# Performance work log

Measured on AMD Instinct MI355X. Metric: run time of the kernel, lower is better.

The kernel has to match this reference:

```python
import jax, jax.numpy as jnp
import numpy as np

N, E, D_IN, D_E, H, OUT, L = 16384, 131072, 128, 64, 256, 16, 4
EPS_MSG = 1e-7   # GENConv message epsilon
EPS_SM = 1e-16   # PyG softmax denominator epsilon


def _ln(x, g, b, eps=1e-5):
    mu = x.mean(-1, keepdims=True)
    var = x.var(-1, keepdims=True)
    return (x - mu) * jax.lax.rsqrt(var + eps) * g + b


def _genconv(x, src, dst, e, w1, b1, lng, lnb, w2, b2, t):
    # message: relu(x_j + edge_attr) + eps  -> [E, H]
    msg = jax.nn.relu(x[src] + e) + EPS_MSG
    # learnable-temperature segment softmax over incoming edges, per feature
    m = msg * t
    mx = jax.ops.segment_max(m, dst, num_segments=N)
    mx = jnp.where(jnp.isfinite(mx), mx, 0.0)  # empty segments -> 0
    ex = jnp.exp(m - mx[dst])
    den = jax.ops.segment_sum(ex, dst, num_segments=N)
    alpha = ex / (den[dst] + EPS_SM)
    agg = jax.ops.segment_sum(msg * alpha, dst, num_segments=N)  # [N, H]
    # root residual then 2-layer MLP: Linear -> LayerNorm -> ReLU -> Linear
    out = agg + x
    h = jax.nn.relu(_ln(out @ w1 + b1, lng, lnb))
    return h @ w2 + b2


def setup_inputs() -> dict:
    key = jax.random.key(0)
    ks = jax.random.split(key, 10)
    gl = lambda k, shape, fan: jax.random.normal(k, shape, jnp.float32) / np.sqrt(fan).astype(np.float32)
    return {
        "x": jax.random.normal(ks[0], (N, D_IN), jnp.float32),
        "edge_index": jax.random.randint(ks[1], (2, E), 0, N, dtype=jnp.int32),
        "edge_attr": jax.random.normal(ks[2], (E, D_E), jnp.float32),
        "enc_w": gl(ks[3], (D_IN, H), D_IN), "enc_b": jnp.zeros((H,), jnp.float32),
        "ee_w": gl(ks[4], (D_E, H), D_E), "ee_b": jnp.zeros((H,), jnp.float32),
        "w1": gl(ks[5], (L, H, 2 * H), H), "b1": jnp.zeros((L, 2 * H), jnp.float32),
        "lng": jnp.ones((L, 2 * H), jnp.float32), "lnb": jnp.zeros((L, 2 * H), jnp.float32),
        "w2": gl(ks[6], (L, 2 * H, H), 2 * H), "b2": jnp.zeros((L, H), jnp.float32),
        "t": jnp.ones((L,), jnp.float32),
        "ng": jnp.ones((L, H), jnp.float32), "nb": jnp.zeros((L, H), jnp.float32),
        "lin_w": gl(ks[7], (H, OUT), H), "lin_b": jnp.zeros((OUT,), jnp.float32),
    }


def reference(x, edge_index, edge_attr, enc_w, enc_b, ee_w, ee_b,
              w1, b1, lng, lnb, w2, b2, t, ng, nb, lin_w, lin_b):
    src, dst = edge_index[0], edge_index[1]
    h = x @ enc_w + enc_b                      # node encoder
    e = edge_attr @ ee_w + ee_b                # edge encoder
    # first layer: conv only (per source forward)
    h = _genconv(h, src, dst, e, w1[0], b1[0], lng[0], lnb[0], w2[0], b2[0], t[0])
    # remaining layers: res+ block = x + conv(relu(norm(x)))  (dropout off in eval)
    for i in range(1, L):
        z = jax.nn.relu(_ln(h, ng[i], nb[i]))
        h = h + _genconv(z, src, dst, e, w1[i], b1[i], lng[i], lnb[i], w2[i], b2[i], t[i])
    h = jax.nn.relu(_ln(h, ng[0], nb[0]))      # layers[0].act(layers[0].norm(x))
    return h @ lin_w + lin_b
```

## Files before the change

kernel.cpp:

```cpp
#include <hip/hip_runtime.h>
#include <stdint.h>
#include <math.h>


typedef __bf16 bf16x8 __attribute__((ext_vector_type(8)));
typedef __bf16 bf16x4 __attribute__((ext_vector_type(4)));
typedef float  f32x4  __attribute__((ext_vector_type(4)));

constexpr int NN   = 16384;
constexpr int NE   = 131072;
constexpr int DIN  = 128;
constexpr int DE   = 64;
constexpr int HD   = 256;
constexpr int HD2  = 512;

__device__ __forceinline__ void gl_lds16(const __bf16* g, __bf16* l) {
  __builtin_amdgcn_global_load_lds((const __attribute__((address_space(1))) void*)g,
                                   (__attribute__((address_space(3))) void*)l, 16, 0, 0);
}

__global__ __launch_bounds__(1024) void k_scan(const int* __restrict__ deg,
                                               int* __restrict__ row_start) {
  __shared__ int part[1024];
  const int t = threadIdx.x;
  const int base = t * 16;
  int loc[16];
  int s = 0;
  #pragma unroll
  for (int i = 0; i < 16; i++) { loc[i] = s; s += deg[base + i]; }
  part[t] = s;
  __syncthreads();
  for (int off = 1; off < 1024; off <<= 1) {
    int v = (t >= off) ? part[t - off] : 0;
    __syncthreads();
    part[t] += v;
    __syncthreads();
  }
  const int excl = (t == 0) ? 0 : part[t - 1];
  #pragma unroll
  for (int i = 0; i < 16; i++) row_start[base + i] = excl + loc[i];
}

__global__ void k_scatter(const int* __restrict__ src, const int* __restrict__ dst,
                          const int* __restrict__ row_start, int* __restrict__ cursor,
                          int2* __restrict__ csr_es) {
  int e = blockIdx.x * 256 + threadIdx.x;
  if (e >= NE) return;
  const int d = dst[e];
  const int p = atomicAdd(&cursor[d], 1);
  csr_es[row_start[d] + p] = make_int2(e, src[e]);
}

__global__ __launch_bounds__(256)
void k_sortw(const int* __restrict__ row_start, const int* __restrict__ deg,
             int2* __restrict__ csr_es, int* __restrict__ posmap) {
  const int wv   = threadIdx.x >> 6;
  const int lane = threadIdx.x & 63;
  const int node = blockIdx.x * 4 + wv;
  if (node >= NN) return;
  const int st = __builtin_amdgcn_readfirstlane(row_start[node]);
  const int dg = __builtin_amdgcn_readfirstlane(deg[node]);
  if (dg <= 1) {
    if (dg == 1 && lane == 0) posmap[csr_es[st].x] = st;
    return;
  }
  if (dg <= 64) {
    int2 pr = make_int2(0x7fffffff, 0);
    if (lane < dg) pr = csr_es[st + lane];
    int rank = 0;
    for (int j = 0; j < dg; j++) {
      const int ej = __builtin_amdgcn_readlane(pr.x, j);
      if (lane < dg && ej < pr.x) rank++;
    }
    if (lane < dg) {
      csr_es[st + rank] = pr;
      posmap[pr.x] = st + rank;
    }
  } else if (lane == 0) {
    for (int a = 1; a < dg; a++) {
      int2 k = csr_es[st + a];
      int b = a - 1;
      while (b >= 0 && csr_es[st + b].x > k.x) { csr_es[st + b + 1] = csr_es[st + b]; b--; }
      csr_es[st + b + 1] = k;
    }
    for (int a = 0; a < dg; a++) posmap[csr_es[st + a].x] = st + a;
  }
}

__global__ void k_prep(const float* __restrict__ enc_w, const float* __restrict__ ee_w,
                       const float* __restrict__ w1, const float* __restrict__ w2,
                       const int* __restrict__ dst, int* __restrict__ deg,
                       __bf16* __restrict__ enc_wT, __bf16* __restrict__ ee_wT,
                       __bf16* __restrict__ w1T, __bf16* __restrict__ w2T) {
  int i = blockIdx.x * 256 + threadIdx.x;
  const int S0 = DIN * HD, S1 = DE * HD, S2 = 4 * HD * HD2, S3 = 4 * HD2 * HD;
  if (i < S0) { int k = i / HD, n = i % HD; enc_wT[n * DIN + k] = (__bf16)enc_w[i]; return; }
  i -= S0;
  if (i < S1) { int k = i / HD, n = i % HD; ee_wT[n * DE + k] = (__bf16)ee_w[i]; return; }
  i -= S1;
  if (i < S2) {
    int l = i / (HD * HD2), r = i % (HD * HD2), k = r / HD2, n = r % HD2;
    w1T[(size_t)l * HD * HD2 + (size_t)n * HD + k] = (__bf16)w1[i]; return;
  }
  i -= S2;
  if (i < S3) {
    int l = i / (HD2 * HD), r = i % (HD2 * HD), k = r / HD, n = r % HD;
    w2T[(size_t)l * HD2 * HD + (size_t)n * HD2 + k] = (__bf16)w2[i]; return;
  }
  i -= S3;
  if (i < NE) { atomicAdd(&deg[dst[i]], 1); return; }
}

template <int RES, int OBF, int STATS, int ESCAT, int AF32>
__global__ __launch_bounds__(256, 3)
void k_gemm(const void* __restrict__ Ap, const __bf16* __restrict__ BT,
            const float* __restrict__ bias, const float* __restrict__ R,
            float* __restrict__ Cf, __bf16* __restrict__ Cb,
            const int* __restrict__ posmap, float2* __restrict__ pstats,
            int M, int Nn, int K) {
  __shared__ __attribute__((aligned(16))) char smem[49152];
  float (*sm)[129] = (float(*)[129])smem;
  float* sbias     = (float*)(smem + 16512);
  float2 (*pst4)[32] = (float2(*)[32])(smem + 17024);
  const __bf16* Ab = (const __bf16*)Ap;
  const float*  Af = (const float*)Ap;
  const int tid  = threadIdx.x;
  const int lane = tid & 63;
  const int wave = tid >> 6;
  const int ntn  = Nn >> 7;
  const int bid  = (int)blockIdx.x;
  const int bn   = (bid >> 3) % ntn;
  const int bm   = (bid & 7) + ((bid >> 3) / ntn) * 8;
  const size_t row0 = (size_t)bm * 128, col0 = (size_t)bn * 128;
  const int wr = (wave >> 1) * 64, wc = (wave & 1) * 64;
  const int ks = lane >> 4, fr = lane & 15;

  auto bufA = [&](int i) -> __bf16* { return (__bf16*)(smem + i * 8192); };
  auto bufB = [&](int i) -> __bf16* { return (__bf16*)(smem + 24576 + i * 8192); };

  f32x4 acc[4][4] = {};

  const int arow = tid >> 2;
  const int aksg = (tid & 3) ^ ((arow >> 1) & 3);

  auto stageB = [&](__bf16* lb, int k0) {
    gl_lds16(BT + (col0 + arow) * K + k0 + aksg * 8, &lb[tid * 8]);
    gl_lds16(BT + (col0 + arow + 64) * K + k0 + aksg * 8, &lb[(tid + 256) * 8]);
  };
  auto stageA = [&](__bf16* la, int k0) {
    gl_lds16(Ab + (row0 + arow) * K + k0 + aksg * 8, &la[tid * 8]);
    gl_lds16(Ab + (row0 + arow + 64) * K + k0 + aksg * 8, &la[(tid + 256) * 8]);
  };
  float4 p0, p1, q0, q1;
  auto loadAf = [&](int k0) {
    const float* a0p = &Af[(row0 + arow) * K + k0 + aksg * 8];
    const float* a1p = &Af[(row0 + arow + 64) * K + k0 + aksg * 8];
    p0 = *(const float4*)a0p; p1 = *(const float4*)(a0p + 4);
    q0 = *(const float4*)a1p; q1 = *(const float4*)(a1p + 4);
  };
  auto writeAf = [&](__bf16* la) {
    bf16x8 o0, o1;
    o0[0] = (__bf16)p0.x; o0[1] = (__bf16)p0.y; o0[2] = (__bf16)p0.z; o0[3] = (__bf16)p0.w;
    o0[4] = (__bf16)p1.x; o0[5] = (__bf16)p1.y; o0[6] = (__bf16)p1.z; o0[7] = (__bf16)p1.w;
    o1[0] = (__bf16)q0.x; o1[1] = (__bf16)q0.y; o1[2] = (__bf16)q0.z; o1[3] = (__bf16)q0.w;
    o1[4] = (__bf16)q1.x; o1[5] = (__bf16)q1.y; o1[6] = (__bf16)q1.z; o1[7] = (__bf16)q1.w;
    *(bf16x8*)&la[tid * 8] = o0;
    *(bf16x8*)&la[(tid + 256) * 8] = o1;
  };

  int slA[4], slB[4];
  #pragma unroll
  for (int m = 0; m < 4; m++) {
    const int rm = wr + m * 16 + fr;
    slA[m] = rm * 4 + (ks ^ ((rm >> 1) & 3));
    const int cn = wc + m * 16 + fr;
    slB[m] = cn * 4 + (ks ^ ((cn >> 1) & 3));
  }

  const int nk = K / 32;
  if (AF32) { loadAf(0); stageB(bufB(0), 0); writeAf(bufA(0)); }
  else      { stageA(bufA(0), 0); stageB(bufB(0), 0); }
  if (nk > 1) {
    if (AF32) { loadAf(32); stageB(bufB(1), 32); writeAf(bufA(1)); }
    else      { stageA(bufA(1), 32); stageB(bufB(1), 32); }
  }
  for (int t = 0; t < nk; t++) {
    const int rem = nk - 1 - t;
    const int nb3 = (t + 2) % 3;
    if (rem >= 2) {
      if (AF32) { loadAf((t + 2) * 32); stageB(bufB(nb3), (t + 2) * 32); }
      else      { stageA(bufA(nb3), (t + 2) * 32); stageB(bufB(nb3), (t + 2) * 32); }
    }
    if (AF32) {
      if (rem >= 2)      asm volatile("s_waitcnt vmcnt(8) lgkmcnt(0)" ::: "memory");
      else if (rem == 1) asm volatile("s_waitcnt vmcnt(2) lgkmcnt(0)" ::: "memory");
      else               asm volatile("s_waitcnt vmcnt(0) lgkmcnt(0)" ::: "memory");
    } else {
      if (rem >= 2)      asm volatile("s_waitcnt vmcnt(8)" ::: "memory");
      else if (rem == 1) asm volatile("s_waitcnt vmcnt(4)" ::: "memory");
      else               asm volatile("s_waitcnt vmcnt(0)" ::: "memory");
    }
    __builtin_amdgcn_s_barrier();
    __builtin_amdgcn_sched_barrier(0);
    const __bf16* la = bufA(t % 3);
    const __bf16* lb = bufB(t % 3);
    bf16x8 af[4], bfr[4];
    #pragma unroll
    for (int m = 0; m < 4; m++) af[m]  = *(const bf16x8*)&la[slA[m] * 8];
    #pragma unroll
    for (int n = 0; n < 4; n++) bfr[n] = *(const bf16x8*)&lb[slB[n] * 8];
    #pragma unroll
    for (int m = 0; m < 4; m++)
      #pragma unroll
      for (int n = 0; n < 4; n++)
        acc[m][n] = __builtin_amdgcn_mfma_f32_16x16x32_bf16(af[m], bfr[n], acc[m][n], 0, 0, 0);
    if (AF32 && rem >= 2) writeAf(bufA(nb3));
    __builtin_amdgcn_s_barrier();
  }
  __syncthreads();

  if (tid < 128) sbias[tid] = bias[col0 + tid];
  const int rbase = (wave >> 1) * 16 + ks * 4;
  const int rr = tid >> 3, cs = (tid & 7) * 16;
  #pragma unroll
  for (int m = 0; m < 4; m++) {
    if (m) __syncthreads();
    #pragma unroll
    for (int n = 0; n < 4; n++)
      #pragma unroll
      for (int r = 0; r < 4; r++)
        sm[rbase + r][wc + n * 16 + fr] = acc[m][n][r];
    __syncthreads();
    const size_t lrow = ((rr & 16) ? 64 : 0) + m * 16 + (rr & 15);
    const size_t grow = row0 + lrow;
    float v[16];
    #pragma unroll
    for (int j = 0; j < 16; j++) v[j] = sm[rr][cs + j] + sbias[cs + j];
    if (STATS) {
      float ssum = 0.f, ssq = 0.f;
      #pragma unroll
      for (int j = 0; j < 16; j++) { ssum += v[j]; ssq += v[j] * v[j]; }
      #pragma unroll
      for (int o = 1; o < 8; o <<= 1) {
        ssum += __shfl_xor(ssum, o);
        ssq  += __shfl_xor(ssq, o);
      }
      if ((tid & 7) == 0) pst4[m][rr].x = ssum, pst4[m][rr].y = ssq;
    }
    const size_t gbase = grow * Nn + col0 + cs;
    if (RES) {
      #pragma unroll
      for (int j = 0; j < 16; j += 4) {
        const float4 rv = *(const float4*)&R[gbase + j];
        v[j] += rv.x; v[j + 1] += rv.y; v[j + 2] += rv.z; v[j + 3] += rv.w;
      }
    }
    if (OBF == 0 || OBF == 2) {
      #pragma unroll
      for (int j = 0; j < 16; j += 4) {
        float4 o; o.x = v[j]; o.y = v[j + 1]; o.z = v[j + 2]; o.w = v[j + 3];
        *(float4*)&Cf[gbase + j] = o;
      }
    }
    if (OBF == 1 || OBF == 2) {
      const size_t crow = ESCAT ? (size_t)posmap[grow] : grow;
      const size_t cbase = crow * Nn + col0 + cs;
      bf16x8 o0, o1;
      #pragma unroll
      for (int j = 0; j < 8; j++) { o0[j] = (__bf16)v[j]; o1[j] = (__bf16)v[8 + j]; }
      *(bf16x8*)&Cb[cbase] = o0;
      *(bf16x8*)&Cb[cbase + 8] = o1;
    }
  }
  if (STATS) {
    __syncthreads();
    if (tid < 128) {
      const int lr = tid;
      const int hi = lr >> 6, m2 = (lr >> 4) & 3, rl = lr & 15;
      pstats[(row0 + lr) * ntn + bn] = pst4[m2][(hi << 4) | rl];
    }
  }
}

template <int RES>
__global__ __launch_bounds__(256, 3)
void k_gemm2(const __bf16* __restrict__ c1b, const __bf16* __restrict__ BT,
             const float* __restrict__ bias, const float* __restrict__ R,
             const float2* __restrict__ pstats, const float* __restrict__ gamma,
             const float* __restrict__ beta, float* __restrict__ Cf, int Nn) {
  constexpr int K = HD2;
  __shared__ __attribute__((aligned(16))) char smem[5120 + 49152];
  float* smu  = (float*)smem;
  float* sinv = (float*)(smem + 512);
  float* sg   = (float*)(smem + 1024);
  float* sb   = (float*)(smem + 3072);
  float (*sm)[129] = (float(*)[129])(smem + 5120);
  float* sbias     = (float*)(smem + 5120 + 16512);
  const int tid  = threadIdx.x;
  const int lane = tid & 63;
  const int wave = tid >> 6;
  const int ntn  = Nn >> 7;
  const int bid  = (int)blockIdx.x;
  const int bn   = (bid >> 3) % ntn;
  const int bm   = (bid & 7) + ((bid >> 3) / ntn) * 8;
  const size_t row0 = (size_t)bm * 128, col0 = (size_t)bn * 128;
  const int wr = (wave >> 1) * 64, wc = (wave & 1) * 64;
  const int ks = lane >> 4, fr = lane & 15;

  auto bufA = [&](int i) -> __bf16* { return (__bf16*)(smem + 5120 + i * 8192); };
  auto bufB = [&](int i) -> __bf16* { return (__bf16*)(smem + 5120 + 24576 + i * 8192); };

  if (tid < 128) {
    const float4* pp = (const float4*)&pstats[(row0 + tid) * 4];
    const float4 a0 = pp[0], a1 = pp[1];
    const float su = a0.x + a0.z + a1.x + a1.z;
    const float sq = a0.y + a0.w + a1.y + a1.w;
    const float mu = su * (1.f / K);
    const float var = sq * (1.f / K) - mu * mu;
    smu[tid] = mu;
    sinv[tid] = rsqrtf(var + 1e-5f);
  }
  sg[tid] = gamma[tid]; sg[tid + 256] = gamma[tid + 256];
  sb[tid] = beta[tid];  sb[tid + 256] = beta[tid + 256];
  __syncthreads();

  const int arow = tid >> 2;
  const int aksg = (tid & 3) ^ ((arow >> 1) & 3);
  const float muA = smu[arow],      ivA = sinv[arow];
  const float muB = smu[arow + 64], ivB = sinv[arow + 64];
  f32x4 acc[4][4] = {};

  auto stageB = [&](__bf16* lb, int k0) {
    gl_lds16(BT + (col0 + arow) * K + k0 + aksg * 8, &lb[tid * 8]);
    gl_lds16(BT + (col0 + arow + 64) * K + k0 + aksg * 8, &lb[(tid + 256) * 8]);
  };
  auto loadA = [&](int k0, bf16x8& a0, bf16x8& a1v) {
    a0  = *(const bf16x8*)&c1b[(row0 + arow) * K + k0 + aksg * 8];
    a1v = *(const bf16x8*)&c1b[(row0 + arow + 64) * K + k0 + aksg * 8];
  };
  auto writeA = [&](__bf16* la, int k0, const bf16x8& a0, const bf16x8& a1v) {
    const int kb = k0 + aksg * 8;
    bf16x8 o0, o1;
    #pragma unroll
    for (int j = 0; j < 8; j++) {
      const float f0 = ((float)a0[j]  - muA) * ivA * sg[kb + j] + sb[kb + j];
      const float f1 = ((float)a1v[j] - muB) * ivB * sg[kb + j] + sb[kb + j];
      o0[j] = (__bf16)fmaxf(f0, 0.f);
      o1[j] = (__bf16)fmaxf(f1, 0.f);
    }
    *(bf16x8*)&la[tid * 8] = o0;
    *(bf16x8*)&la[(tid + 256) * 8] = o1;
  };

  int slA[4], slB[4];
  #pragma unroll
  for (int m = 0; m < 4; m++) {
    const int rm = wr + m * 16 + fr;
    slA[m] = rm * 4 + (ks ^ ((rm >> 1) & 3));
    const int cn = wc + m * 16 + fr;
    slB[m] = cn * 4 + (ks ^ ((cn >> 1) & 3));
  }

  const int nk = K / 32;
  {
    bf16x8 a0, a1v;
    loadA(0, a0, a1v);
    stageB(bufB(0), 0);
    writeA(bufA(0), 0, a0, a1v);
    loadA(32, a0, a1v);
    stageB(bufB(1), 32);
    writeA(bufA(1), 32, a0, a1v);
  }
  for (int t = 0; t < nk; t++) {
    const int rem = nk - 1 - t;
    const int nb3 = (t + 2) % 3;
    bf16x8 a0, a1v;
    if (rem >= 2) {
      stageB(bufB(nb3), (t + 2) * 32);
      loadA((t + 2) * 32, a0, a1v);
    }
    if (rem >= 2)      asm volatile("s_waitcnt vmcnt(6) lgkmcnt(0)" ::: "memory");
    else if (rem == 1) asm volatile("s_waitcnt vmcnt(2) lgkmcnt(0)" ::: "memory");
    else               asm volatile("s_waitcnt vmcnt(0) lgkmcnt(0)" ::: "memory");
    __builtin_amdgcn_s_barrier();
    __builtin_amdgcn_sched_barrier(0);
    const __bf16* la = bufA(t % 3);
    const __bf16* lb = bufB(t % 3);
    bf16x8 af[4], bfr[4];
    #pragma unroll
    for (int m = 0; m < 4; m++) af[m]  = *(const bf16x8*)&la[slA[m] * 8];
    #pragma unroll
    for (int n = 0; n < 4; n++) bfr[n] = *(const bf16x8*)&lb[slB[n] * 8];
    #pragma unroll
    for (int m = 0; m < 4; m++)
      #pragma unroll
      for (int n = 0; n < 4; n++)
        acc[m][n] = __builtin_amdgcn_mfma_f32_16x16x32_bf16(af[m], bfr[n], acc[m][n], 0, 0, 0);
    if (rem >= 2) writeA(bufA(nb3), (t + 2) * 32, a0, a1v);
    __builtin_amdgcn_s_barrier();
  }
  __syncthreads();

  if (tid < 128) sbias[tid] = bias[col0 + tid];
  const int rbase = (wave >> 1) * 16 + ks * 4;
  const int rr = tid >> 3, cs = (tid & 7) * 16;
  #pragma unroll
  for (int m = 0; m < 4; m++) {
    if (m) __syncthreads();
    #pragma unroll
    for (int n = 0; n < 4; n++)
      #pragma unroll
      for (int r = 0; r < 4; r++)
        sm[rbase + r][wc + n * 16 + fr] = acc[m][n][r];
    __syncthreads();
    const size_t grow = row0 + ((rr & 16) ? 64 : 0) + m * 16 + (rr & 15);
    const size_t gbase = grow * Nn + col0 + cs;
    float v[16];
    #pragma unroll
    for (int j = 0; j < 16; j++) v[j] = sm[rr][cs + j] + sbias[cs + j];
    if (RES) {
      #pragma unroll
      for (int j = 0; j < 16; j += 4) {
        const float4 rv = *(const float4*)&R[gbase + j];
        v[j] += rv.x; v[j + 1] += rv.y; v[j + 2] += rv.z; v[j + 3] += rv.w;
      }
    }
    #pragma unroll
    for (int j = 0; j < 16; j += 4) {
      float4 o; o.x = v[j]; o.y = v[j + 1]; o.z = v[j + 2]; o.w = v[j + 3];
      *(float4*)&Cf[gbase + j] = o;
    }
  }
}

__global__ __launch_bounds__(256)
void k_msg(const __bf16* __restrict__ zb, const __bf16* __restrict__ ecsr,
           const int* __restrict__ row_start, const int* __restrict__ deg,
           const int2* __restrict__ csr_es, const float* __restrict__ tvec,
           int layer, __bf16* __restrict__ a1) {
  const int wv   = __builtin_amdgcn_readfirstlane(threadIdx.x >> 6);
  const int lane = threadIdx.x & 63;
  const int node = blockIdx.x * 4 + wv;
  const int st = __builtin_amdgcn_readfirstlane(row_start[node]);
  const int dg = __builtin_amdgcn_readfirstlane(deg[node]);
  const float t = tvec[layer];
  const int f0 = lane * 4;

  int my_src = 0;
  if (lane < dg) my_src = csr_es[st + lane].y;
  const bf16x4 sv = *(const bf16x4*)&zb[(size_t)node * HD + f0];

  float den[4] = {0.f, 0.f, 0.f, 0.f}, agg[4] = {0.f, 0.f, 0.f, 0.f};
  const int dmain = dg < 64 ? dg : 64;
  int j = 0;
  for (; j + 8 <= dmain; j += 8) {
    bf16x4 zv[8], ev[8];
    #pragma unroll
    for (int u = 0; u < 8; u++) {
      const int sn = __builtin_amdgcn_readlane(my_src, j + u);
      zv[u] = *(const bf16x4*)&zb[(size_t)sn * HD + f0];
      ev[u] = *(const bf16x4*)&ecsr[(size_t)(st + j + u) * HD + f0];
    }
    #pragma unroll
    for (int u = 0; u < 8; u++)
      #pragma unroll
      for (int q = 0; q < 4; q++) {
        const float m  = fmaxf((float)zv[u][q] + (float)ev[u][q], 0.f) + 1e-7f;
        const float ex = __expf(m * t);
        den[q] += ex;
        agg[q] += m * ex;
      }
  }
  for (; j + 4 <= dmain; j += 4) {
    bf16x4 zv[4], ev[4];
    #pragma unroll
    for (int u = 0; u < 4; u++) {
      const int sn = __builtin_amdgcn_readlane(my_src, j + u);
      zv[u] = *(const bf16x4*)&zb[(size_t)sn * HD + f0];
      ev[u] = *(const bf16x4*)&ecsr[(size_t)(st + j + u) * HD + f0];
    }
    #pragma unroll
    for (int u = 0; u < 4; u++)
      #pragma unroll
      for (int q = 0; q < 4; q++) {
        const float m  = fmaxf((float)zv[u][q] + (float)ev[u][q], 0.f) + 1e-7f;
        const float ex = __expf(m * t);
        den[q] += ex;
        agg[q] += m * ex;
      }
  }
  for (; j < dmain; j++) {
    const int sn = __builtin_amdgcn_readlane(my_src, j);
    const bf16x4 zv = *(const bf16x4*)&zb[(size_t)sn * HD + f0];
    const bf16x4 ev = *(const bf16x4*)&ecsr[(size_t)(st + j) * HD + f0];
    #pragma unroll
    for (int q = 0; q < 4; q++) {
      const float m  = fmaxf((float)zv[q] + (float)ev[q], 0.f) + 1e-7f;
      const float ex = __expf(m * t);
      den[q] += ex;
      agg[q] += m * ex;
    }
  }
  for (int jj = 64; jj < dg; jj++) {
    const int2 pr = csr_es[st + jj];
    const bf16x4 zv = *(const bf16x4*)&zb[(size_t)pr.y * HD + f0];
    const bf16x4 ev = *(const bf16x4*)&ecsr[(size_t)(st + jj) * HD + f0];
    #pragma unroll
    for (int q = 0; q < 4; q++) {
      const float m  = fmaxf((float)zv[q] + (float)ev[q], 0.f) + 1e-7f;
      const float ex = __expf(m * t);
      den[q] += ex;
      agg[q] += m * ex;
    }
  }
  bf16x4 r;
  #pragma unroll
  for (int q = 0; q < 4; q++) {
    const float res = (dg > 0) ? agg[q] / (den[q] + 1e-16f) : 0.f;
    r[q] = (__bf16)(res + (float)sv[q]);
  }
  *(bf16x4*)&a1[(size_t)node * HD + f0] = r;
}

__global__ __launch_bounds__(256)
void k_prenorm(const float* __restrict__ h, const float* __restrict__ g,
               const float* __restrict__ b, __bf16* __restrict__ zb) {
  const int row  = blockIdx.x * 4 + (threadIdx.x >> 6);
  const int lane = threadIdx.x & 63;
  const float4 v = *(const float4*)&h[(size_t)row * HD + lane * 4];
  float s = v.x + v.y + v.z + v.w;
  for (int o = 1; o < 64; o <<= 1) s += __shfl_xor(s, o);
  const float mu = s * (1.f / HD);
  const float dx = v.x - mu, dy = v.y - mu, dz = v.z - mu, dw = v.w - mu;
  float q = dx * dx + dy * dy + dz * dz + dw * dw;
  for (int o = 1; o < 64; o <<= 1) q += __shfl_xor(q, o);
  const float inv = rsqrtf(q * (1.f / HD) + 1e-5f);
  const float4 gv = *(const float4*)&g[lane * 4];
  const float4 bv = *(const float4*)&b[lane * 4];
  bf16x4 r;
  r[0] = (__bf16)fmaxf(dx * inv * gv.x + bv.x, 0.f);
  r[1] = (__bf16)fmaxf(dy * inv * gv.y + bv.y, 0.f);
  r[2] = (__bf16)fmaxf(dz * inv * gv.z + bv.z, 0.f);
  r[3] = (__bf16)fmaxf(dw * inv * gv.w + bv.w, 0.f);
  *(bf16x4*)&zb[(size_t)row * HD + lane * 4] = r;
}

__global__ __launch_bounds__(256)
void k_headln(const float* __restrict__ h, const float* __restrict__ g,
              const float* __restrict__ b, const float* __restrict__ lw,
              const float* __restrict__ lb, float* __restrict__ out) {
  __shared__ float slw[256 * 16];
  __shared__ float srow[16 * 256];
  const int t = threadIdx.x;
  const size_t row0 = (size_t)blockIdx.x * 16;
  #pragma unroll
  for (int j = 0; j < 16; j++) slw[j * 256 + t] = lw[j * 256 + t];
  const int rl = t >> 4, col = t & 15;
  float v[16];
  float s = 0.f, sq = 0.f;
  #pragma unroll
  for (int j = 0; j < 16; j += 4) {
    const float4 hv = *(const float4*)&h[(row0 + rl) * HD + col * 16 + j];
    v[j] = hv.x; v[j + 1] = hv.y; v[j + 2] = hv.z; v[j + 3] = hv.w;
  }
  #pragma unroll
  for (int j = 0; j < 16; j++) { s += v[j]; sq += v[j] * v[j]; }
  #pragma unroll
  for (int o = 1; o < 16; o <<= 1) { s += __shfl_xor(s, o); sq += __shfl_xor(sq, o); }
  const float mu = s * (1.f / HD);
  const float inv = rsqrtf(sq * (1.f / HD) - mu * mu + 1e-5f);
  #pragma unroll
  for (int j = 0; j < 16; j += 4) {
    const float4 gv = *(const float4*)&g[col * 16 + j];
    const float4 bv = *(const float4*)&b[col * 16 + j];
    srow[rl * 256 + col * 16 + j]     = fmaxf((v[j]     - mu) * inv * gv.x + bv.x, 0.f);
    srow[rl * 256 + col * 16 + j + 1] = fmaxf((v[j + 1] - mu) * inv * gv.y + bv.y, 0.f);
    srow[rl * 256 + col * 16 + j + 2] = fmaxf((v[j + 2] - mu) * inv * gv.z + bv.z, 0.f);
    srow[rl * 256 + col * 16 + j + 3] = fmaxf((v[j + 3] - mu) * inv * gv.w + bv.w, 0.f);
  }
  __syncthreads();
  float acc = lb[col];
  #pragma unroll 8
  for (int k = 0; k < 256; k++) acc += srow[rl * 256 + k] * slw[k * 16 + col];
  out[(row0 + rl) * 16 + col] = acc;
}

extern "C" void kernel_launch(void* const* d_in, const int* in_sizes, int n_in,
                              void* d_out, int out_size, void* d_ws, size_t ws_size,
                              hipStream_t stream) {
  const float* x     = (const float*)d_in[0];
  const int*   ei    = (const int*)d_in[1];
  const float* ea    = (const float*)d_in[2];
  const float* enc_w = (const float*)d_in[3];
  const float* enc_b = (const float*)d_in[4];
  const float* ee_w  = (const float*)d_in[5];
  const float* ee_b  = (const float*)d_in[6];
  const float* w1    = (const float*)d_in[7];
  const float* b1    = (const float*)d_in[8];
  const float* lng   = (const float*)d_in[9];
  const float* lnb   = (const float*)d_in[10];
  const float* w2    = (const float*)d_in[11];
  const float* b2    = (const float*)d_in[12];
  const float* tvec  = (const float*)d_in[13];
  const float* ng    = (const float*)d_in[14];
  const float* nb    = (const float*)d_in[15];
  const float* lin_w = (const float*)d_in[16];
  const float* lin_b = (const float*)d_in[17];

  uint8_t* p = (uint8_t*)d_ws;
  auto alloc = [&](size_t bytes) { uint8_t* r = p; p += (bytes + 255) & ~(size_t)255; return r; };
  __bf16* e_csr  = (__bf16*)alloc((size_t)NE * HD * 2);
  float*  h      = (float*) alloc((size_t)NN * HD * 4);
  __bf16* hb     = (__bf16*)alloc((size_t)NN * HD * 2);
  __bf16* zb     = (__bf16*)alloc((size_t)NN * HD * 2);
  __bf16* a1     = (__bf16*)alloc((size_t)NN * HD * 2);
  __bf16* c1b    = (__bf16*)alloc((size_t)NN * HD2 * 2);
  float2* pstats = (float2*)alloc((size_t)NN * 4 * 8);
  __bf16* enc_wT = (__bf16*)alloc((size_t)HD * DIN * 2);
  __bf16* ee_wT  = (__bf16*)alloc((size_t)HD * DE * 2);
  __bf16* w1T    = (__bf16*)alloc((size_t)4 * HD2 * HD * 2);
  __bf16* w2T    = (__bf16*)alloc((size_t)4 * HD * HD2 * 2);
  int* deg       = (int*)alloc((size_t)NN * 4);
  int* cursor    = (int*)alloc((size_t)NN * 4);
  int* row_start = (int*)alloc((size_t)NN * 4);
  int* posmap    = (int*)alloc((size_t)NE * 4);
  int2* csr_es   = (int2*)alloc((size_t)NE * 8);

  const int* srcp = ei;
  const int* dstp = ei + NE;

  hipMemsetAsync(deg, 0, (size_t)NN * 8, stream);

  const int prep_total = DIN * HD + DE * HD + 4 * HD * HD2 + 4 * HD2 * HD + NE;
  k_prep<<<(prep_total + 255) / 256, 256, 0, stream>>>(enc_w, ee_w, w1, w2, dstp, deg,
                                                       enc_wT, ee_wT, w1T, w2T);
  k_scan<<<1, 1024, 0, stream>>>(deg, row_start);
  k_scatter<<<NE / 256, 256, 0, stream>>>(srcp, dstp, row_start, cursor, csr_es);
  k_sortw<<<NN / 4, 256, 0, stream>>>(row_start, deg, csr_es, posmap);

  k_gemm<0, 2, 0, 0, 1><<<(NN / 128) * (HD / 128), 256, 0, stream>>>(
      x, enc_wT, enc_b, nullptr, h, hb, nullptr, nullptr, NN, HD, DIN);
  k_gemm<0, 1, 0, 1, 1><<<(NE / 128) * (HD / 128), 256, 0, stream>>>(
      ea, ee_wT, ee_b, nullptr, nullptr, e_csr, posmap, nullptr, NE, HD, DE);

  for (int i = 0; i < 4; i++) {
    const __bf16* zin = (i == 0) ? hb : zb;
    k_msg<<<NN / 4, 256, 0, stream>>>(zin, e_csr, row_start, deg, csr_es, tvec, i, a1);
    k_gemm<0, 1, 1, 0, 0><<<(NN / 128) * (HD2 / 128), 256, 0, stream>>>(
        a1, w1T + (size_t)i * HD2 * HD, b1 + (size_t)i * HD2, nullptr, nullptr, c1b,
        nullptr, pstats, NN, HD2, HD);
    if (i == 0)
      k_gemm2<0><<<(NN / 128) * (HD / 128), 256, 0, stream>>>(
          c1b, w2T + (size_t)i * HD * HD2, b2 + (size_t)i * HD, nullptr, pstats,
          lng + (size_t)i * HD2, lnb + (size_t)i * HD2, h, HD);
    else
      k_gemm2<1><<<(NN / 128) * (HD / 128), 256, 0, stream>>>(
          c1b, w2T + (size_t)i * HD * HD2, b2 + (size_t)i * HD, h, pstats,
          lng + (size_t)i * HD2, lnb + (size_t)i * HD2, h, HD);
    if (i < 3)
      k_prenorm<<<NN / 4, 256, 0, stream>>>(h, ng + (size_t)(i + 1) * HD,
                                            nb + (size_t)(i + 1) * HD, zb);
  }

  k_headln<<<NN / 16, 256, 0, stream>>>(h, ng, nb, lin_w, lin_b, (float*)d_out);
}
```

Before: 338.6 us.

## Fuse residual LayerNorm+ReLU into second GEMM epilogue with full-row tiles

The second MLP GEMM now has each block compute a full 32x256 output row tile, so the epilogue can compute the row LayerNorm+ReLU and write the bf16 z input for the next layer directly. This removes the separate prenorm kernel and the final fp32 h re-read in the head, which now consumes bf16 z. The trade-off is a smaller M tile (32 rows) with a double buffer instead of a triple buffer, so B is reloaded per 32 rows and only half the threads load A. The head's final matmul input is also quantized to bf16.

```diff
diff --git a/kernel.cpp b/kernel.cpp
--- a/kernel.cpp
+++ b/kernel.cpp
@@ -282,154 +282,166 @@
   }
 }
 
-template <int RES>
+template <int RES, int WH>
 __global__ __launch_bounds__(256, 3)
-void k_gemm2(const __bf16* __restrict__ c1b, const __bf16* __restrict__ BT,
-             const float* __restrict__ bias, const float* __restrict__ R,
-             const float2* __restrict__ pstats, const float* __restrict__ gamma,
-             const float* __restrict__ beta, float* __restrict__ Cf, int Nn) {
+void k_gemm2f(const __bf16* __restrict__ c1b, const __bf16* __restrict__ BT,
+              const float* __restrict__ bias, const float* __restrict__ R,
+              const float2* __restrict__ pstats, const float* __restrict__ gamma,
+              const float* __restrict__ beta, const float* __restrict__ g2,
+              const float* __restrict__ b2, float* __restrict__ hout,
+              __bf16* __restrict__ zout) {
   constexpr int K = HD2;
-  __shared__ __attribute__((aligned(16))) char smem[5120 + 49152];
+  constexpr int NC = HD;
+  __shared__ __attribute__((aligned(16))) char smem[7424 + 36864];
   float* smu  = (float*)smem;
-  float* sinv = (float*)(smem + 512);
-  float* sg   = (float*)(smem + 1024);
-  float* sb   = (float*)(smem + 3072);
-  float (*sm)[129] = (float(*)[129])(smem + 5120);
-  float* sbias     = (float*)(smem + 5120 + 16512);
-  const int tid  = threadIdx.x;
-  const int lane = tid & 63;
-  const int wave = tid >> 6;
-  const int ntn  = Nn >> 7;
-  const int bid  = (int)blockIdx.x;
-  const int bn   = (bid >> 3) % ntn;
-  const int bm   = (bid & 7) + ((bid >> 3) / ntn) * 8;
-  const size_t row0 = (size_t)bm * 128, col0 = (size_t)bn * 128;
-  const int wr = (wave >> 1) * 64, wc = (wave & 1) * 64;
+  float* sinv = (float*)(smem + 128);
+  float* sg   = (float*)(smem + 256);
+  float* sb   = (float*)(smem + 2304);
+  float* sg2  = (float*)(smem + 4352);
+  float* sb2  = (float*)(smem + 5376);
+  float* sbias= (float*)(smem + 6400);
+  char* arena = smem + 7424;
+  auto bufA = [&](int i) -> __bf16* { return (__bf16*)(arena + i * 18432); };
+  auto bufB = [&](int i) -> __bf16* { return (__bf16*)(arena + i * 18432 + 2048); };
+  float (*sm)[264] = (float(*)[264])arena;
+
+  const int tid = threadIdx.x, lane = tid & 63, wave = tid >> 6;
+  const size_t row0 = (size_t)blockIdx.x * 32;
+  const int wc = wave * 64;
   const int ks = lane >> 4, fr = lane & 15;
 
-  auto bufA = [&](int i) -> __bf16* { return (__bf16*)(smem + 5120 + i * 8192); };
-  auto bufB = [&](int i) -> __bf16* { return (__bf16*)(smem + 5120 + 24576 + i * 8192); };
-
-  if (tid < 128) {
+  if (tid < 32) {
     const float4* pp = (const float4*)&pstats[(row0 + tid) * 4];
     const float4 a0 = pp[0], a1 = pp[1];
     const float su = a0.x + a0.z + a1.x + a1.z;
     const float sq = a0.y + a0.w + a1.y + a1.w;
     const float mu = su * (1.f / K);
-    const float var = sq * (1.f / K) - mu * mu;
     smu[tid] = mu;
-    sinv[tid] = rsqrtf(var + 1e-5f);
+    sinv[tid] = rsqrtf(sq * (1.f / K) - mu * mu + 1e-5f);
   }
   sg[tid] = gamma[tid]; sg[tid + 256] = gamma[tid + 256];
   sb[tid] = beta[tid];  sb[tid + 256] = beta[tid + 256];
+  sg2[tid] = g2[tid]; sb2[tid] = b2[tid]; sbias[tid] = bias[tid];
   __syncthreads();
 
   const int arow = tid >> 2;
-  const int aksg = (tid & 3) ^ ((arow >> 1) & 3);
-  const float muA = smu[arow],      ivA = sinv[arow];
-  const float muB = smu[arow + 64], ivB = sinv[arow + 64];
-  f32x4 acc[4][4] = {};
+  const int akg  = (tid & 3) ^ ((arow >> 1) & 3);
+  f32x4 acc[2][4] = {};
+  bf16x8 aReg;
 
   auto stageB = [&](__bf16* lb, int k0) {
-    gl_lds16(BT + (col0 + arow) * K + k0 + aksg * 8, &lb[tid * 8]);
-    gl_lds16(BT + (col0 + arow + 64) * K + k0 + aksg * 8, &lb[(tid + 256) * 8]);
+    #pragma unroll
+    for (int j = 0; j < 4; j++) {
+      const int s = j * 256 + tid;
+      const int scol = s >> 2;
+      const int kg = (s & 3) ^ ((scol >> 1) & 3);
+      gl_lds16(BT + (size_t)scol * K + k0 + kg * 8, &lb[s * 8]);
+    }
   };
-  auto loadA = [&](int k0, bf16x8& a0, bf16x8& a1v) {
-    a0  = *(const bf16x8*)&c1b[(row0 + arow) * K + k0 + aksg * 8];
-    a1v = *(const bf16x8*)&c1b[(row0 + arow + 64) * K + k0 + aksg * 8];
+  auto loadA = [&](int k0) {
+    if (tid < 128) aReg = *(const bf16x8*)&c1b[(row0 + arow) * K + k0 + akg * 8];
   };
-  auto writeA = [&](__bf16* la, int k0, const bf16x8& a0, const bf16x8& a1v) {
-    const int kb = k0 + aksg * 8;
-    bf16x8 o0, o1;
-    #pragma unroll
-    for (int j = 0; j < 8; j++) {
-      const float f0 = ((float)a0[j]  - muA) * ivA * sg[kb + j] + sb[kb + j];
-      const float f1 = ((float)a1v[j] - muB) * ivB * sg[kb + j] + sb[kb + j];
-      o0[j] = (__bf16)fmaxf(f0, 0.f);
-      o1[j] = (__bf16)fmaxf(f1, 0.f);
-    }
-    *(bf16x8*)&la[tid * 8] = o0;
-    *(bf16x8*)&la[(tid + 256) * 8] = o1;
+  auto writeA = [&](__bf16* la, int k0) {
+    if (tid < 128) {
+      const int kb = k0 + akg * 8;
+      const float mu = smu[arow], iv = sinv[arow];
+      bf16x8 o;
+      #pragma unroll
+      for (int j = 0; j < 8; j++) {
+        const float f = ((float)aReg[j] - mu) * iv * sg[kb + j] + sb[kb + j];
+        o[j] = (__bf16)fmaxf(f, 0.f);
+      }
+      *(bf16x8*)&la[tid * 8] = o;
+    }
   };
 
-  int slA[4], slB[4];
-  #pragma unroll
-  for (int m = 0; m < 4; m++) {
-    const int rm = wr + m * 16 + fr;
+  int slA[2], slB[4];
+  #pragma unroll
+  for (int m = 0; m < 2; m++) {
+    const int rm = m * 16 + fr;
     slA[m] = rm * 4 + (ks ^ ((rm >> 1) & 3));
-    const int cn = wc + m * 16 + fr;
-    slB[m] = cn * 4 + (ks ^ ((cn >> 1) & 3));
+  }
+  #pragma unroll
+  for (int n = 0; n < 4; n++) {
+    const int cn = wc + n * 16 + fr;
+    slB[n] = cn * 4 + (ks ^ ((cn >> 1) & 3));
   }
 
   const int nk = K / 32;
-  {
-    bf16x8 a0, a1v;
-    loadA(0, a0, a1v);
-    stageB(bufB(0), 0);
-    writeA(bufA(0), 0, a0, a1v);
-    loadA(32, a0, a1v);
-    stageB(bufB(1), 32);
-    writeA(bufA(1), 32, a0, a1v);
-  }
+  loadA(0); stageB(bufB(0), 0); writeA(bufA(0), 0);
   for (int t = 0; t < nk; t++) {
-    const int rem = nk - 1 - t;
-    const int nb3 = (t + 2) % 3;
-    bf16x8 a0, a1v;
-    if (rem >= 2) {
-      stageB(bufB(nb3), (t + 2) * 32);
-      loadA((t + 2) * 32, a0, a1v);
-    }
-    if (rem >= 2)      asm volatile("s_waitcnt vmcnt(6) lgkmcnt(0)" ::: "memory");
-    else if (rem == 1) asm volatile("s_waitcnt vmcnt(2) lgkmcnt(0)" ::: "memory");
-    else               asm volatile("s_waitcnt vmcnt(0) lgkmcnt(0)" ::: "memory");
+    const bool more = (t + 1 < nk);
+    const int cur = t & 1;
+    if (more) { stageB(bufB(cur ^ 1), (t + 1) * 32); loadA((t + 1) * 32); }
+    if (more) {
+      if (wave < 2) asm volatile("s_waitcnt vmcnt(5) lgkmcnt(0)" ::: "memory");
+      else          asm volatile("s_waitcnt vmcnt(4) lgkmcnt(0)" ::: "memory");
+    } else {
+      asm volatile("s_waitcnt vmcnt(0) lgkmcnt(0)" ::: "memory");
+    }
     __builtin_amdgcn_s_barrier();
     __builtin_amdgcn_sched_barrier(0);
-    const __bf16* la = bufA(t % 3);
-    const __bf16* lb = bufB(t % 3);
-    bf16x8 af[4], bfr[4];
-    #pragma unroll
-    for (int m = 0; m < 4; m++) af[m]  = *(const bf16x8*)&la[slA[m] * 8];
+    const __bf16* la = bufA(cur);
+    const __bf16* lb = bufB(cur);
+    bf16x8 af[2], bfr[4];
+    #pragma unroll
+    for (int m = 0; m < 2; m++) af[m]  = *(const bf16x8*)&la[slA[m] * 8];
     #pragma unroll
     for (int n = 0; n < 4; n++) bfr[n] = *(const bf16x8*)&lb[slB[n] * 8];
     #pragma unroll
-    for (int m = 0; m < 4; m++)
+    for (int m = 0; m < 2; m++)
       #pragma unroll
       for (int n = 0; n < 4; n++)
         acc[m][n] = __builtin_amdgcn_mfma_f32_16x16x32_bf16(af[m], bfr[n], acc[m][n], 0, 0, 0);
-    if (rem >= 2) writeA(bufA(nb3), (t + 2) * 32, a0, a1v);
+    if (more) writeA(bufA(cur ^ 1), (t + 1) * 32);
     __builtin_amdgcn_s_barrier();
   }
   __syncthreads();
 
-  if (tid < 128) sbias[tid] = bias[col0 + tid];
-  const int rbase = (wave >> 1) * 16 + ks * 4;
-  const int rr = tid >> 3, cs = (tid & 7) * 16;
-  #pragma unroll
-  for (int m = 0; m < 4; m++) {
-    if (m) __syncthreads();
+  #pragma unroll
+  for (int m = 0; m < 2; m++)
     #pragma unroll
     for (int n = 0; n < 4; n++)
       #pragma unroll
       for (int r = 0; r < 4; r++)
-        sm[rbase + r][wc + n * 16 + fr] = acc[m][n][r];
-    __syncthreads();
-    const size_t grow = row0 + ((rr & 16) ? 64 : 0) + m * 16 + (rr & 15);
-    const size_t gbase = grow * Nn + col0 + cs;
-    float v[16];
-    #pragma unroll
-    for (int j = 0; j < 16; j++) v[j] = sm[rr][cs + j] + sbias[cs + j];
+        sm[m * 16 + ks * 4 + r][wc + n * 16 + fr] = acc[m][n][r];
+  __syncthreads();
+  const int rr = tid >> 3, c0 = (tid & 7) * 4;
+  float v[32];
+  float s = 0.f, sq = 0.f;
+  #pragma unroll
+  for (int j = 0; j < 8; j++) {
+    const int c = c0 + j * 32;
+    float x0 = sm[rr][c]     + sbias[c];
+    float x1 = sm[rr][c + 1] + sbias[c + 1];
+    float x2 = sm[rr][c + 2] + sbias[c + 2];
+    float x3 = sm[rr][c + 3] + sbias[c + 3];
     if (RES) {
-      #pragma unroll
-      for (int j = 0; j < 16; j += 4) {
-        const float4 rv = *(const float4*)&R[gbase + j];
-        v[j] += rv.x; v[j + 1] += rv.y; v[j + 2] += rv.z; v[j + 3] += rv.w;
-      }
-    }
-    #pragma unroll
-    for (int j = 0; j < 16; j += 4) {
-      float4 o; o.x = v[j]; o.y = v[j + 1]; o.z = v[j + 2]; o.w = v[j + 3];
-      *(float4*)&Cf[gbase + j] = o;
-    }
+      const float4 rv = *(const float4*)&R[(row0 + rr) * NC + c];
+      x0 += rv.x; x1 += rv.y; x2 += rv.z; x3 += rv.w;
+    }
+    v[j * 4] = x0; v[j * 4 + 1] = x1; v[j * 4 + 2] = x2; v[j * 4 + 3] = x3;
+    s += x0 + x1 + x2 + x3;
+    sq += x0 * x0 + x1 * x1 + x2 * x2 + x3 * x3;
+  }
+  #pragma unroll
+  for (int o = 1; o < 8; o <<= 1) { s += __shfl_xor(s, o); sq += __shfl_xor(sq, o); }
+  const float mu = s * (1.f / NC);
+  const float inv = rsqrtf(sq * (1.f / NC) - mu * mu + 1e-5f);
+  #pragma unroll
+  for (int j = 0; j < 8; j++) {
+    const int c = c0 + j * 32;
+    if (WH) {
+      float4 o;
+      o.x = v[j * 4]; o.y = v[j * 4 + 1]; o.z = v[j * 4 + 2]; o.w = v[j * 4 + 3];
+      *(float4*)&hout[(row0 + rr) * NC + c] = o;
+    }
+    bf16x4 z;
+    z[0] = (__bf16)fmaxf((v[j * 4]     - mu) * inv * sg2[c]     + sb2[c],     0.f);
+    z[1] = (__bf16)fmaxf((v[j * 4 + 1] - mu) * inv * sg2[c + 1] + sb2[c + 1], 0.f);
+    z[2] = (__bf16)fmaxf((v[j * 4 + 2] - mu) * inv * sg2[c + 2] + sb2[c + 2], 0.f);
+    z[3] = (__bf16)fmaxf((v[j * 4 + 3] - mu) * inv * sg2[c + 3] + sb2[c + 3], 0.f);
+    *(bf16x4*)&zout[(row0 + rr) * NC + c] = z;
   }
 }
 
@@ -523,66 +535,28 @@
 }
 
 __global__ __launch_bounds__(256)
-void k_prenorm(const float* __restrict__ h, const float* __restrict__ g,
-               const float* __restrict__ b, __bf16* __restrict__ zb) {
-  const int row  = blockIdx.x * 4 + (threadIdx.x >> 6);
-  const int lane = threadIdx.x & 63;
-  const float4 v = *(const float4*)&h[(size_t)row * HD + lane * 4];
-  float s = v.x + v.y + v.z + v.w;
-  for (int o = 1; o < 64; o <<= 1) s += __shfl_xor(s, o);
-  const float mu = s * (1.f / HD);
-  const float dx = v.x - mu, dy = v.y - mu, dz = v.z - mu, dw = v.w - mu;
-  float q = dx * dx + dy * dy + dz * dz + dw * dw;
-  for (int o = 1; o < 64; o <<= 1) q += __shfl_xor(q, o);
-  const float inv = rsqrtf(q * (1.f / HD) + 1e-5f);
-  const float4 gv = *(const float4*)&g[lane * 4];
-  const float4 bv = *(const float4*)&b[lane * 4];
-  bf16x4 r;
-  r[0] = (__bf16)fmaxf(dx * inv * gv.x + bv.x, 0.f);
-  r[1] = (__bf16)fmaxf(dy * inv * gv.y + bv.y, 0.f);
-  r[2] = (__bf16)fmaxf(dz * inv * gv.z + bv.z, 0.f);
-  r[3] = (__bf16)fmaxf(dw * inv * gv.w + bv.w, 0.f);
-  *(bf16x4*)&zb[(size_t)row * HD + lane * 4] = r;
-}
-
-__global__ __launch_bounds__(256)
-void k_headln(const float* __restrict__ h, const float* __restrict__ g,
-              const float* __restrict__ b, const float* __restrict__ lw,
-              const float* __restrict__ lb, float* __restrict__ out) {
+void k_head(const __bf16* __restrict__ zb, const float* __restrict__ lw,
+            const float* __restrict__ lb, float* __restrict__ out) {
   __shared__ float slw[256 * 16];
-  __shared__ float srow[16 * 256];
+  __shared__ __bf16 srow[16 * 256];
   const int t = threadIdx.x;
   const size_t row0 = (size_t)blockIdx.x * 16;
   #pragma unroll
   for (int j = 0; j < 16; j++) slw[j * 256 + t] = lw[j * 256 + t];
+  #pragma unroll
+  for (int j = 0; j < 2; j++) {
+    const int c = j * 256 + t;
+    ((bf16x8*)srow)[c] = ((const bf16x8*)(zb + row0 * 256))[c];
+  }
+  __syncthreads();
   const int rl = t >> 4, col = t & 15;
-  float v[16];
-  float s = 0.f, sq = 0.f;
-  #pragma unroll
-  for (int j = 0; j < 16; j += 4) {
-    const float4 hv = *(const float4*)&h[(row0 + rl) * HD + col * 16 + j];
-    v[j] = hv.x; v[j + 1] = hv.y; v[j + 2] = hv.z; v[j + 3] = hv.w;
-  }
-  #pragma unroll
-  for (int j = 0; j < 16; j++) { s += v[j]; sq += v[j] * v[j]; }
-  #pragma unroll
-  for (int o = 1; o < 16; o <<= 1) { s += __shfl_xor(s, o); sq += __shfl_xor(sq, o); }
-  const float mu = s * (1.f / HD);
-  const float inv = rsqrtf(sq * (1.f / HD) - mu * mu + 1e-5f);
-  #pragma unroll
-  for (int j = 0; j < 16; j += 4) {
-    const float4 gv = *(const float4*)&g[col * 16 + j];
-    const float4 bv = *(const float4*)&b[col * 16 + j];
-    srow[rl * 256 + col * 16 + j]     = fmaxf((v[j]     - mu) * inv * gv.x + bv.x, 0.f);
-    srow[rl * 256 + col * 16 + j + 1] = fmaxf((v[j + 1] - mu) * inv * gv.y + bv.y, 0.f);
-    srow[rl * 256 + col * 16 + j + 2] = fmaxf((v[j + 2] - mu) * inv * gv.z + bv.z, 0.f);
-    srow[rl * 256 + col * 16 + j + 3] = fmaxf((v[j + 3] - mu) * inv * gv.w + bv.w, 0.f);
-  }
-  __syncthreads();
-  float acc = lb[col];
-  #pragma unroll 8
-  for (int k = 0; k < 256; k++) acc += srow[rl * 256 + k] * slw[k * 16 + col];
-  out[(row0 + rl) * 16 + col] = acc;
+  float s = lb[col];
+  for (int k0 = 0; k0 < 256; k0 += 8) {
+    const bf16x8 zv = *(const bf16x8*)&srow[rl * 256 + k0];
+    #pragma unroll
+    for (int q = 0; q < 8; q++) s += (float)zv[q] * slw[(k0 + q) * 16 + col];
+  }
+  out[(row0 + rl) * 16 + col] = s;
 }
 
 extern "C" void kernel_launch(void* const* d_in, const int* in_sizes, int n_in,
@@ -649,18 +623,22 @@
     k_gemm<0, 1, 1, 0, 0><<<(NN / 128) * (HD2 / 128), 256, 0, stream>>>(
         a1, w1T + (size_t)i * HD2 * HD, b1 + (size_t)i * HD2, nullptr, nullptr, c1b,
         nullptr, pstats, NN, HD2, HD);
+    const int nidx = (i < 3) ? i + 1 : 0;
+    const float* gg = ng + (size_t)nidx * HD;
+    const float* bb = nb + (size_t)nidx * HD;
     if (i == 0)
-      k_gemm2<0><<<(NN / 128) * (HD / 128), 256, 0, stream>>>(
+      k_gemm2f<0, 1><<<NN / 32, 256, 0, stream>>>(
           c1b, w2T + (size_t)i * HD * HD2, b2 + (size_t)i * HD, nullptr, pstats,
-          lng + (size_t)i * HD2, lnb + (size_t)i * HD2, h, HD);
+          lng + (size_t)i * HD2, lnb + (size_t)i * HD2, gg, bb, h, zb);
+    else if (i < 3)
+      k_gemm2f<1, 1><<<NN / 32, 256, 0, stream>>>(
+          c1b, w2T + (size_t)i * HD * HD2, b2 + (size_t)i * HD, h, pstats,
+          lng + (size_t)i * HD2, lnb + (size_t)i * HD2, gg, bb, h, zb);
     else
-      k_gemm2<1><<<(NN / 128) * (HD / 128), 256, 0, stream>>>(
+      k_gemm2f<1, 0><<<NN / 32, 256, 0, stream>>>(
           c1b, w2T + (size_t)i * HD * HD2, b2 + (size_t)i * HD, h, pstats,
-          lng + (size_t)i * HD2, lnb + (size_t)i * HD2, h, HD);
-    if (i < 3)
-      k_prenorm<<<NN / 4, 256, 0, stream>>>(h, ng + (size_t)(i + 1) * HD,
-                                            nb + (size_t)(i + 1) * HD, zb);
-  }
-
-  k_headln<<<NN / 16, 256, 0, stream>>>(h, ng, nb, lin_w, lin_b, (float*)d_out);
-}
+          lng + (size_t)i * HD2, lnb + (size_t)i * HD2, gg, bb, h, zb);
+  }
+
+  k_head<<<NN / 16, 256, 0, stream>>>(zb, lin_w, lin_b, (float*)d_out);
+}
```

Result: faster. 314.9 us (-7.0%).
